# Performance work log

Measured on AMD Instinct MI355X. Metric: run time of the kernel, lower is better.

## Reference

```python
import jax, jax.numpy as jnp
import numpy as np

N_NODES = 50000
N_EDGES = 800000
N_GRAPHS = 64
PERIOD = 10
HID = 300
NLAYER = 5
EPS = 1e-5


def setup_inputs() -> dict:
    key = jax.random.key(0)
    ks = jax.random.split(key, 16)
    batch = jnp.sort(jax.random.randint(ks[0], (N_NODES,), 0, N_GRAPHS))
    x = jax.random.normal(ks[1], (N_NODES, 2 * PERIOD), dtype=jnp.float32)
    edge_index = jax.random.randint(ks[2], (2, N_EDGES), 0, N_NODES)
    edge_attr = jax.random.normal(ks[3], (N_EDGES,), dtype=jnp.float32)

    def xavier(k, fan_in, fan_out, shape):
        a = float(np.sqrt(6.0 / (fan_in + fan_out)))
        return jax.random.uniform(k, shape, jnp.float32, -a, a)

    linW = xavier(ks[4], 2 * PERIOD, HID, (2 * PERIOD, HID))
    linb = jnp.zeros((HID,), jnp.float32)
    W1s = xavier(ks[5], HID, 2 * HID, (NLAYER, HID, 2 * HID))
    b1s = jnp.zeros((NLAYER, 2 * HID), jnp.float32)
    g1s = jnp.ones((NLAYER, 2 * HID), jnp.float32)
    be1s = jnp.zeros((NLAYER, 2 * HID), jnp.float32)
    W2s = xavier(ks[6], 2 * HID, HID, (NLAYER, 2 * HID, HID))
    b2s = jnp.zeros((NLAYER, HID), jnp.float32)
    gos = jnp.ones((NLAYER, HID), jnp.float32)
    bos = jnp.zeros((NLAYER, HID), jnp.float32)
    return {"batch": batch, "x": x, "edge_index": edge_index, "edge_attr": edge_attr,
            "linW": linW, "linb": linb, "W1s": W1s, "b1s": b1s, "g1s": g1s,
            "be1s": be1s, "W2s": W2s, "b2s": b2s, "gos": gos, "bos": bos}


def _bn(h, g, b):
    # training-mode BatchNorm1d: batch mean, biased variance
    m = jnp.mean(h, axis=0)
    v = jnp.var(h, axis=0)
    return g * (h - m) * jax.lax.rsqrt(v + EPS) + b


def reference(batch, x, edge_index, edge_attr, linW, linb, W1s, b1s, g1s, be1s, W2s, b2s, gos, bos):
    src, dst = edge_index[0], edge_index[1]
    ew = edge_attr[:, None]  # [E,1]
    h = x @ linW + linb  # [N, HID]
    for i in range(NLAYER):
        # gather-modulate-scatter message passing (sign=False: message = w * x_j)
        msg = ew * h[src]  # [E, HID]
        agg = jax.ops.segment_sum(msg, dst, num_segments=N_NODES)  # [N, HID]
        # inner MLP with BatchNorm
        t = agg @ W1s[i] + b1s[i]  # [N, 2*HID]
        t = jax.nn.relu(_bn(t, g1s[i], be1s[i]))
        t = t @ W2s[i] + b2s[i]  # [N, HID]
        # outer BatchNorm
        h = _bn(t, gos[i], bos[i])
        if i != NLAYER - 1:
            h = jax.nn.relu(h)
    xpool = jax.ops.segment_sum(h, batch, num_segments=N_GRAPHS)  # [G, HID]
    return (h, xpool)
```

## Files before the change

kernel.cpp:

```cpp
#include <hip/hip_runtime.h>
#include <hip/hip_fp16.h>
#include <stdint.h>

typedef _Float16 f16x8 __attribute__((ext_vector_type(8)));
typedef unsigned short u16x8 __attribute__((ext_vector_type(8)));
typedef float f32x4 __attribute__((ext_vector_type(4)));

constexpr int NN  = 50000;
constexpr int NE  = 800000;
constexpr int NG  = 64;
constexpr int H   = 300;
constexpr int H2  = 600;
constexpr int IND = 20;
constexpr int NL  = 5;

constexpr int MP  = 50048;
constexpr int KP1 = 320;
constexpr int KP2 = 608;
constexpr int NP1 = 640;
constexpr int NP2 = 384;
constexpr int HCS = 320;

constexpr int SCAN_B = (NN + 1023) / 1024;

static __device__ __forceinline__ ushort f2h(float f) {
  return __half_as_ushort(__float2half(f));
}
static __device__ __forceinline__ float h2f_lo(uint32_t u) {
  return __half2float(__ushort_as_half((ushort)(u & 0xFFFFu)));
}
static __device__ __forceinline__ float h2f_hi(uint32_t u) {
  return __half2float(__ushort_as_half((ushort)(u >> 16)));
}
static __device__ __forceinline__ uint32_t packh(float a, float b) {
  return (uint32_t)f2h(a) | ((uint32_t)f2h(b) << 16);
}

static __device__ __forceinline__ f16x8 relu8(f16x8 t) {
#if __has_builtin(__builtin_elementwise_max)
  f16x8 z = 0;
  return __builtin_elementwise_max(t, z);
#else
  u16x8 u = *reinterpret_cast<u16x8*>(&t);
  u = u & (u16x8)((u >> 15) - (unsigned short)1);
  return *reinterpret_cast<f16x8*>(&u);
#endif
}


__global__ void hist_kernel(const int* __restrict__ dst, int* __restrict__ hist) {
  int i = blockIdx.x * blockDim.x + threadIdx.x;
  if (i < NE) atomicAdd(&hist[dst[i]], 1);
}

__global__ __launch_bounds__(1024) void scan1_kernel(const int* __restrict__ hist,
                                                     int* __restrict__ offs,
                                                     int* __restrict__ bsum) {
  __shared__ int sdata[1024];
  int b = blockIdx.x, tid = threadIdx.x;
  int i = b * 1024 + tid;
  int v = (i < NN) ? hist[i] : 0;
  sdata[tid] = v;
  __syncthreads();
  for (int ofs = 1; ofs < 1024; ofs <<= 1) {
    int t = (tid >= ofs) ? sdata[tid - ofs] : 0;
    __syncthreads();
    sdata[tid] += t;
    __syncthreads();
  }
  if (i < NN) offs[i] = sdata[tid] - v;
  if (tid == 1023) bsum[b] = sdata[1023];
}

__global__ void scan2_kernel(const int* __restrict__ bsum, int* __restrict__ bpre) {
  if (threadIdx.x == 0) {
    int run = 0;
    for (int b = 0; b < SCAN_B; ++b) {
      bpre[b] = run;
      run += bsum[b];
    }
    bpre[SCAN_B] = run;
  }
}

__global__ __launch_bounds__(1024) void scan3_kernel(const int* __restrict__ bpre,
                                                     int* __restrict__ offs,
                                                     int* __restrict__ cursor) {
  int b = blockIdx.x, tid = threadIdx.x;
  int i = b * 1024 + tid;
  if (i < NN) {
    int o = offs[i] + bpre[b];
    offs[i] = o;
    cursor[i] = o;
  }
  if (i == 0) offs[NN] = bpre[SCAN_B];
}

__global__ void scatter_kernel(const int* __restrict__ src, const int* __restrict__ dst,
                               const float* __restrict__ w, int* __restrict__ cursor,
                               int* __restrict__ ssrc, float* __restrict__ sw) {
  int i = blockIdx.x * blockDim.x + threadIdx.x;
  if (i < NE) {
    int d = dst[i];
    int p = atomicAdd(&cursor[d], 1);
    ssrc[p] = src[i];
    sw[p]   = w[i];
  }
}


__global__ void padzero_kernel(ushort* __restrict__ b, int KPAD, int Ntrue) {
  long long nA = (long long)(MP - NN) * KPAD;
  int padc = KPAD - Ntrue;
  long long nB = (long long)NN * padc;
  long long total = nA + nB;
  long long stride = (long long)gridDim.x * blockDim.x;
  for (long long i = blockIdx.x * (long long)blockDim.x + threadIdx.x; i < total; i += stride) {
    long long off;
    if (i < nA) {
      off = (long long)NN * KPAD + i;
    } else {
      long long j = i - nA;
      long long r = j / padc;
      long long c = Ntrue + (j - r * padc);
      off = r * KPAD + c;
    }
    b[off] = 0;
  }
}


__global__ void packW1_kernel(const float* __restrict__ W1s, ushort* __restrict__ Wp) {
  int idx = blockIdx.x * blockDim.x + threadIdx.x;
  if (idx >= NL * NP1 * KP1) return;
  int i = idx / (NP1 * KP1);
  int rem = idx - i * (NP1 * KP1);
  int n = rem / KP1;
  int k = rem - n * KP1;
  float v = (n < H2 && k < H) ? W1s[((long long)i * H + k) * H2 + n] : 0.f;
  Wp[idx] = f2h(v);
}

__global__ void packW2_kernel(const float* __restrict__ W2s, ushort* __restrict__ Wp) {
  int idx = blockIdx.x * blockDim.x + threadIdx.x;
  if (idx >= NL * NP2 * KP2) return;
  int i = idx / (NP2 * KP2);
  int rem = idx - i * (NP2 * KP2);
  int n = rem / KP2;
  int k = rem - n * KP2;
  float v = (n < H && k < H2) ? W2s[((long long)i * H2 + k) * H + n] : 0.f;
  Wp[idx] = f2h(v);
}


__global__ __launch_bounds__(256) void lin_kernel(const float* __restrict__ x,
                                                  const float* __restrict__ W,
                                                  const float* __restrict__ b,
                                                  ushort* __restrict__ hc) {
  __shared__ float Ws[IND * H];
  __shared__ float bs[H];
  int tid = threadIdx.x;
  for (int i = tid; i < IND * H; i += 256) Ws[i] = W[i];
  for (int i = tid; i < H; i += 256) bs[i] = b[i];
  __syncthreads();
  const int QPR = H / 4;
  int total = NN * QPR;
  for (int idx = blockIdx.x * 256 + tid; idx < total; idx += gridDim.x * 256) {
    int n = idx / QPR;
    int f = (idx - n * QPR) * 4;
    float a0 = bs[f], a1 = bs[f + 1], a2 = bs[f + 2], a3 = bs[f + 3];
    const float* xr = x + n * IND;
#pragma unroll
    for (int k = 0; k < IND; ++k) {
      float xv = xr[k];
      const float* wk = &Ws[k * H + f];
      a0 = fmaf(xv, wk[0], a0);
      a1 = fmaf(xv, wk[1], a1);
      a2 = fmaf(xv, wk[2], a2);
      a3 = fmaf(xv, wk[3], a3);
    }
    uint2 o = make_uint2(packh(a0, a1), packh(a2, a3));
    *reinterpret_cast<uint2*>(hc + (long long)n * HCS + f) = o;
  }
}


__global__ __launch_bounds__(192) void agg_kernel(const ushort* __restrict__ hc,
                                                  const int* __restrict__ offs,
                                                  const int* __restrict__ ssrc,
                                                  const float* __restrict__ sw,
                                                  ushort* __restrict__ agg) {
  int n = blockIdx.x;
  int t = threadIdx.x;
  if (t >= H / 2) return;
  int s = offs[n], e = offs[n + 1];
  float a0 = 0.f, a1 = 0.f;
  int i = s;
  for (; i + 7 < e; i += 8) {
    uint32_t u[8];
    float w[8];
#pragma unroll
    for (int j = 0; j < 8; ++j) {
      int sn = ssrc[i + j];
      w[j] = sw[i + j];
      u[j] = *reinterpret_cast<const uint32_t*>(hc + (long long)sn * HCS + 2 * t);
    }
#pragma unroll
    for (int j = 0; j < 8; ++j) {
      a0 = fmaf(w[j], h2f_lo(u[j]), a0);
      a1 = fmaf(w[j], h2f_hi(u[j]), a1);
    }
  }
  for (; i < e; ++i) {
    int sn = ssrc[i];
    float w = sw[i];
    uint32_t u = *reinterpret_cast<const uint32_t*>(hc + (long long)sn * HCS + 2 * t);
    a0 = fmaf(w, h2f_lo(u), a0);
    a1 = fmaf(w, h2f_hi(u), a1);
  }
  *reinterpret_cast<uint32_t*>(agg + (long long)n * KP1 + 2 * t) = packh(a0, a1);
}


template <bool FUSE_BN>
__global__ __launch_bounds__(256, 4) void gemm_mfma(
    const ushort* __restrict__ A, const ushort* __restrict__ Bp,
    const float* __restrict__ bias, ushort* __restrict__ C,
    float* __restrict__ sum, float* __restrict__ sq,
    int M, int Ntrue, int Ktiles, int KPAD, int Cstride, int ntiles,
    const ushort* __restrict__ bns, const ushort* __restrict__ bnh) {
  __shared__ ushort AL[2][128 * 32];
  int nwg = gridDim.x;
  int hw = blockIdx.x;
  int xcd = hw & 7, slot = hw >> 3;
  int q = nwg >> 3, r = nwg & 7;
  int logical = (xcd < r ? xcd * (q + 1) : r * (q + 1) + (xcd - r) * q) + slot;
  int mt = logical / ntiles;
  int nt = logical - mt * ntiles;

  int tid = threadIdx.x;
  int lane = tid & 63, wid = tid >> 6;
  int wm = wid >> 1, wn = wid & 1;
  int lm = lane & 15, lg = lane >> 4;
  long long bm = (long long)mt * 128;
  long long bn = (long long)nt * 128;

  int srow = lane >> 2;
  int slotc = lane & 3;

  const ushort* Bb = Bp + (bn + wn * 64 + lm) * KPAD + lg * 8;

  f32x4 acc[4][4] = {};

  auto stageA = [&](int buf, int kt) {
    int k0 = kt * 32;
#pragma unroll
    for (int j = 0; j < 2; ++j) {
      int row = j * 64 + wid * 16 + srow;
      int cg = slotc ^ ((row >> 1) & 3);
      long long go = (bm + row) * KPAD + k0 + cg * 8;
      ushort* l = &AL[buf][(j * 64 + wid * 16) * 32];
      __builtin_amdgcn_global_load_lds(
          (const __attribute__((address_space(1))) void*)(A + go),
          (__attribute__((address_space(3))) void*)l, 16, 0, 0);
    }
  };

  f16x8 bcur[4], bnxt[4];
  stageA(0, 0);
#pragma unroll
  for (int i = 0; i < 4; ++i)
    bcur[i] = *reinterpret_cast<const f16x8*>(Bb + (long long)i * 16 * KPAD);
  __syncthreads();

  for (int kt = 0; kt < Ktiles; ++kt) {
    int cur = kt & 1;
    int nk = kt + 1;
    if (nk < Ktiles) {
      stageA(nk & 1, nk);
#pragma unroll
      for (int i = 0; i < 4; ++i)
        bnxt[i] = *reinterpret_cast<const f16x8*>(Bb + (long long)i * 16 * KPAD + nk * 32);
    }
    f16x8 a[4];
#pragma unroll
    for (int i = 0; i < 4; ++i) {
      int row = wm * 64 + i * 16 + lm;
      int c = lg ^ ((row >> 1) & 3);
      a[i] = *reinterpret_cast<const f16x8*>(&AL[cur][row * 32 + c * 8]);
    }
    if constexpr (FUSE_BN) {
      int kbase = kt * 32 + lg * 8;
      f16x8 sv = *reinterpret_cast<const f16x8*>(bns + kbase);
      f16x8 hv = *reinterpret_cast<const f16x8*>(bnh + kbase);
#pragma unroll
      for (int i = 0; i < 4; ++i) a[i] = relu8(a[i] * sv + hv);
    }
#pragma unroll
    for (int mf = 0; mf < 4; ++mf)
#pragma unroll
      for (int nf = 0; nf < 4; ++nf)
        acc[mf][nf] = __builtin_amdgcn_mfma_f32_16x16x32_f16(a[mf], bcur[nf], acc[mf][nf], 0, 0, 0);
    __syncthreads();
#pragma unroll
    for (int i = 0; i < 4; ++i) bcur[i] = bnxt[i];
  }

  int colb = (int)bn + wn * 64 + lm;
#pragma unroll
  for (int nf = 0; nf < 4; ++nf) {
    int col = colb + nf * 16;
    bool cok = col < Ntrue;
    float bv = cok ? bias[col] : 0.f;
    float cs = 0.f, cq = 0.f;
#pragma unroll
    for (int mf = 0; mf < 4; ++mf) {
      int row0 = (int)bm + wm * 64 + mf * 16 + lg * 4;
      f32x4 v = acc[mf][nf];
#pragma unroll
      for (int e = 0; e < 4; ++e) {
        float w = v[e] + bv;
        bool ok = cok && (row0 + e < M);
        if (ok) {
          cs += w;
          cq = fmaf(w, w, cq);
        }
        float wp = __shfl_xor(w, 1);
        if (ok && ((lm & 1) == 0)) {
          *reinterpret_cast<uint32_t*>(&C[(long long)(row0 + e) * Cstride + col]) = packh(w, wp);
        }
      }
    }
    cs += __shfl_xor(cs, 16);
    cq += __shfl_xor(cq, 16);
    cs += __shfl_xor(cs, 32);
    cq += __shfl_xor(cq, 32);
    if (lg == 0 && cok) {
      atomicAdd(&sum[col], cs);
      atomicAdd(&sq[col], cq);
    }
  }
}


__global__ void finalize_kernel(const float* __restrict__ sum, const float* __restrict__ sq,
                                const float* __restrict__ g, const float* __restrict__ be,
                                int C, int Calloc, float invM, float* __restrict__ scale,
                                float* __restrict__ shift, ushort* __restrict__ scaleh,
                                ushort* __restrict__ shifth) {
  int c = blockIdx.x * blockDim.x + threadIdx.x;
  if (c >= Calloc) return;
  float sc = 0.f, sh = 0.f;
  if (c < C) {
    float m = sum[c] * invM;
    float v = sq[c] * invM - m * m;
    sc = g[c] * rsqrtf(v + 1e-5f);
    sh = be[c] - m * sc;
  }
  scale[c] = sc;
  shift[c] = sh;
  if (scaleh) {
    scaleh[c] = f2h(sc);
    shifth[c] = f2h(sh);
  }
}

template <bool LAST>
__global__ void bn2_kernel(const ushort* __restrict__ u_, const float* __restrict__ scale,
                           const float* __restrict__ shift, ushort* __restrict__ hc,
                           float* __restrict__ out) {
  const int QPR = H / 4;
  int total = NN * QPR;
  for (int idx = blockIdx.x * blockDim.x + threadIdx.x; idx < total;
       idx += gridDim.x * blockDim.x) {
    int r = idx / QPR;
    int c = (idx - r * QPR) * 4;
    uint2 u = *reinterpret_cast<const uint2*>(u_ + (long long)r * KP1 + c);
    float4 sc = *reinterpret_cast<const float4*>(scale + c);
    float4 sh = *reinterpret_cast<const float4*>(shift + c);
    float w0 = fmaf(h2f_lo(u.x), sc.x, sh.x);
    float w1 = fmaf(h2f_hi(u.x), sc.y, sh.y);
    float w2 = fmaf(h2f_lo(u.y), sc.z, sh.z);
    float w3 = fmaf(h2f_hi(u.y), sc.w, sh.w);
    if (LAST) {
      *reinterpret_cast<float4*>(out + (long long)r * H + c) = make_float4(w0, w1, w2, w3);
    } else {
      w0 = fmaxf(w0, 0.f);
      w1 = fmaxf(w1, 0.f);
      w2 = fmaxf(w2, 0.f);
      w3 = fmaxf(w3, 0.f);
      *reinterpret_cast<uint2*>(hc + (long long)r * HCS + c) =
          make_uint2(packh(w0, w1), packh(w2, w3));
    }
  }
}


__global__ void bounds_kernel(const int* __restrict__ batch, int* __restrict__ gstart) {
  int g = threadIdx.x;
  if (g > NG) return;
  if (g == NG) { gstart[NG] = NN; return; }
  int lo = 0, hi = NN;
  while (lo < hi) {
    int mid = (lo + hi) >> 1;
    if (batch[mid] < g) lo = mid + 1; else hi = mid;
  }
  gstart[g] = lo;
}

__global__ __launch_bounds__(320) void pool_kernel(const float* __restrict__ h,
                                                   const int* __restrict__ gstart,
                                                   float* __restrict__ xpool) {
  int g = blockIdx.x;
  int f = threadIdx.x;
  if (f >= H) return;
  int s = gstart[g], e = gstart[g + 1];
  float acc = 0.f;
  for (int r = s + blockIdx.y; r < e; r += gridDim.y) acc += h[(long long)r * H + f];
  atomicAdd(&xpool[g * H + f], acc);
}


extern "C" void kernel_launch(void* const* d_in, const int* in_sizes, int n_in,
                              void* d_out, int out_size, void* d_ws, size_t ws_size,
                              hipStream_t stream) {
  const int*   batch = (const int*)d_in[0];
  const float* x     = (const float*)d_in[1];
  const int*   eidx  = (const int*)d_in[2];
  const float* eattr = (const float*)d_in[3];
  const float* linW  = (const float*)d_in[4];
  const float* linb  = (const float*)d_in[5];
  const float* W1s   = (const float*)d_in[6];
  const float* b1s   = (const float*)d_in[7];
  const float* g1s   = (const float*)d_in[8];
  const float* be1s  = (const float*)d_in[9];
  const float* W2s   = (const float*)d_in[10];
  const float* b2s   = (const float*)d_in[11];
  const float* gos   = (const float*)d_in[12];
  const float* bos   = (const float*)d_in[13];

  const int* esrc = eidx;
  const int* edst = eidx + NE;

  char* p = (char*)d_ws;
  auto alloc = [&](size_t bytes) {
    char* r = p;
    p += (bytes + 255) & ~(size_t)255;
    return r;
  };
  ushort* tb   = (ushort*)alloc((size_t)MP * KP2 * 2);
  ushort* ub   = (ushort*)alloc((size_t)MP * KP1 * 2);
  ushort* hc   = (ushort*)alloc((size_t)NN * HCS * 2);
  ushort* W1p  = (ushort*)alloc((size_t)NL * NP1 * KP1 * 2);
  ushort* W2p  = (ushort*)alloc((size_t)NL * NP2 * KP2 * 2);
  int*    hist   = (int*)alloc((size_t)NN * 4);
  int*    offs   = (int*)alloc((size_t)(NN + 64) * 4);
  int*    cursor = (int*)alloc((size_t)NN * 4);
  int*    ssrc   = (int*)alloc((size_t)NE * 4);
  float*  sw     = (float*)alloc((size_t)NE * 4);
  int*    bsum   = (int*)alloc((size_t)(SCAN_B + 1) * 4);
  int*    bpre   = (int*)alloc((size_t)(SCAN_B + 1) * 4);
  float*  sum1   = (float*)alloc((size_t)(H2 * 2 + H * 2) * 4);
  float*  sq1    = sum1 + H2;
  float*  sum2   = sq1 + H2;
  float*  sq2    = sum2 + H;
  float*  scale1 = (float*)alloc((size_t)(KP2 * 2 + H * 2) * 4);
  float*  shift1 = scale1 + KP2;
  float*  scale2 = shift1 + KP2;
  float*  shift2 = scale2 + H;
  ushort* scaleh = (ushort*)alloc((size_t)KP2 * 2 * 2);
  ushort* shifth = scaleh + KP2;
  int*    gstart = (int*)alloc((size_t)(NG + 1) * 4);
  size_t needed = (size_t)(p - (char*)d_ws);
  if (ws_size < needed) return;

  float* hout  = (float*)d_out;
  float* xpool = hout + (long long)NN * H;

  padzero_kernel<<<1024, 256, 0, stream>>>(tb, KP2, H2);
  padzero_kernel<<<1024, 256, 0, stream>>>(ub, KP1, H);

  packW1_kernel<<<(NL * NP1 * KP1 + 255) / 256, 256, 0, stream>>>(W1s, W1p);
  packW2_kernel<<<(NL * NP2 * KP2 + 255) / 256, 256, 0, stream>>>(W2s, W2p);

  hipMemsetAsync(hist, 0, (size_t)NN * 4, stream);
  hist_kernel<<<(NE + 255) / 256, 256, 0, stream>>>(edst, hist);
  scan1_kernel<<<SCAN_B, 1024, 0, stream>>>(hist, offs, bsum);
  scan2_kernel<<<1, 64, 0, stream>>>(bsum, bpre);
  scan3_kernel<<<SCAN_B, 1024, 0, stream>>>(bpre, offs, cursor);
  scatter_kernel<<<(NE + 255) / 256, 256, 0, stream>>>(esrc, edst, eattr, cursor, ssrc, sw);

  lin_kernel<<<4096, 256, 0, stream>>>(x, linW, linb, hc);

  const int MT = MP / 128;
  for (int i = 0; i < NL; ++i) {
    agg_kernel<<<NN, 192, 0, stream>>>(hc, offs, ssrc, sw, ub);
    hipMemsetAsync(sum1, 0, (size_t)(H2 * 2 + H * 2) * 4, stream);

    gemm_mfma<false><<<MT * (NP1 / 128), 256, 0, stream>>>(
        ub, W1p + (size_t)i * NP1 * KP1, b1s + (size_t)i * H2, tb,
        sum1, sq1, NN, H2, KP1 / 32, KP1, KP2, NP1 / 128, nullptr, nullptr);
    finalize_kernel<<<(KP2 + 255) / 256, 256, 0, stream>>>(
        sum1, sq1, g1s + (size_t)i * H2, be1s + (size_t)i * H2, H2, KP2, 1.f / NN,
        scale1, shift1, scaleh, shifth);

    gemm_mfma<true><<<MT * (NP2 / 128), 256, 0, stream>>>(
        tb, W2p + (size_t)i * NP2 * KP2, b2s + (size_t)i * H, ub,
        sum2, sq2, NN, H, KP2 / 32, KP2, KP1, NP2 / 128, scaleh, shifth);
    finalize_kernel<<<(H + 255) / 256, 256, 0, stream>>>(
        sum2, sq2, gos + (size_t)i * H, bos + (size_t)i * H, H, H, 1.f / NN,
        scale2, shift2, nullptr, nullptr);
    if (i < NL - 1) {
      bn2_kernel<false><<<4096, 256, 0, stream>>>(ub, scale2, shift2, hc, hout);
    } else {
      bn2_kernel<true><<<4096, 256, 0, stream>>>(ub, scale2, shift2, hc, hout);
    }
  }

  hipMemsetAsync(xpool, 0, (size_t)NG * H * 4, stream);
  bounds_kernel<<<1, 128, 0, stream>>>(batch, gstart);
  pool_kernel<<<dim3(NG, 8), 320, 0, stream>>>(hout, gstart, xpool);
}
```

Measured before the change: 1.354 ms.

## Switch MFMA GEMM to single-wave 64x64 tiles without workgroup barriers

The fused GEMM kernel moves from a 256-thread workgroup computing a 128x128 tile to a single 64-thread wave computing a 64x64 tile, launched on a correspondingly larger grid. Because each workgroup is one wave, the __syncthreads calls are dropped and explicit s_waitcnt vmcnt instructions order the async global-to-LDS A loads. The register double-buffering of B is removed, so B fragments are loaded in the same iteration they are consumed. This removes barrier stalls and raises the number of independent workgroups, but A tiles are no longer shared across waves through LDS, and B load latency is less hidden.

```diff
diff --git a/kernel.cpp b/kernel.cpp
--- a/kernel.cpp
+++ b/kernel.cpp
@@ -223,13 +223,13 @@
 
 
 template <bool FUSE_BN>
-__global__ __launch_bounds__(256, 4) void gemm_mfma(
+__global__ __launch_bounds__(64, 4) void gemm_mfma(
     const ushort* __restrict__ A, const ushort* __restrict__ Bp,
     const float* __restrict__ bias, ushort* __restrict__ C,
     float* __restrict__ sum, float* __restrict__ sq,
     int M, int Ntrue, int Ktiles, int KPAD, int Cstride, int ntiles,
     const ushort* __restrict__ bns, const ushort* __restrict__ bnh) {
-  __shared__ ushort AL[2][128 * 32];
+  __shared__ ushort AL[2][64 * 32];
   int nwg = gridDim.x;
   int hw = blockIdx.x;
   int xcd = hw & 7, slot = hw >> 3;
@@ -238,54 +238,51 @@
   int mt = logical / ntiles;
   int nt = logical - mt * ntiles;
 
-  int tid = threadIdx.x;
-  int lane = tid & 63, wid = tid >> 6;
-  int wm = wid >> 1, wn = wid & 1;
+  int lane = threadIdx.x & 63;
   int lm = lane & 15, lg = lane >> 4;
-  long long bm = (long long)mt * 128;
-  long long bn = (long long)nt * 128;
+  long long bm = (long long)mt * 64;
+  long long bn = (long long)nt * 64;
 
   int srow = lane >> 2;
   int slotc = lane & 3;
 
-  const ushort* Bb = Bp + (bn + wn * 64 + lm) * KPAD + lg * 8;
+  const ushort* Bb = Bp + (bn + lm) * KPAD + lg * 8;
 
   f32x4 acc[4][4] = {};
 
   auto stageA = [&](int buf, int kt) {
     int k0 = kt * 32;
 #pragma unroll
-    for (int j = 0; j < 2; ++j) {
-      int row = j * 64 + wid * 16 + srow;
+    for (int j = 0; j < 4; ++j) {
+      int row = j * 16 + srow;
       int cg = slotc ^ ((row >> 1) & 3);
       long long go = (bm + row) * KPAD + k0 + cg * 8;
-      ushort* l = &AL[buf][(j * 64 + wid * 16) * 32];
+      ushort* l = &AL[buf][(j * 16) * 32];
       __builtin_amdgcn_global_load_lds(
           (const __attribute__((address_space(1))) void*)(A + go),
           (__attribute__((address_space(3))) void*)l, 16, 0, 0);
     }
   };
 
-  f16x8 bcur[4], bnxt[4];
   stageA(0, 0);
-#pragma unroll
-  for (int i = 0; i < 4; ++i)
-    bcur[i] = *reinterpret_cast<const f16x8*>(Bb + (long long)i * 16 * KPAD);
-  __syncthreads();
 
   for (int kt = 0; kt < Ktiles; ++kt) {
     int cur = kt & 1;
     int nk = kt + 1;
+    f16x8 b[4];
+#pragma unroll
+    for (int i = 0; i < 4; ++i)
+      b[i] = *reinterpret_cast<const f16x8*>(Bb + (long long)i * 16 * KPAD + kt * 32);
     if (nk < Ktiles) {
       stageA(nk & 1, nk);
-#pragma unroll
-      for (int i = 0; i < 4; ++i)
-        bnxt[i] = *reinterpret_cast<const f16x8*>(Bb + (long long)i * 16 * KPAD + nk * 32);
+      asm volatile("s_waitcnt vmcnt(4)" ::: "memory");
+    } else {
+      asm volatile("s_waitcnt vmcnt(0)" ::: "memory");
     }
     f16x8 a[4];
 #pragma unroll
     for (int i = 0; i < 4; ++i) {
-      int row = wm * 64 + i * 16 + lm;
+      int row = i * 16 + lm;
       int c = lg ^ ((row >> 1) & 3);
       a[i] = *reinterpret_cast<const f16x8*>(&AL[cur][row * 32 + c * 8]);
     }
@@ -300,13 +297,10 @@
     for (int mf = 0; mf < 4; ++mf)
 #pragma unroll
       for (int nf = 0; nf < 4; ++nf)
-        acc[mf][nf] = __builtin_amdgcn_mfma_f32_16x16x32_f16(a[mf], bcur[nf], acc[mf][nf], 0, 0, 0);
-    __syncthreads();
-#pragma unroll
-    for (int i = 0; i < 4; ++i) bcur[i] = bnxt[i];
-  }
-
-  int colb = (int)bn + wn * 64 + lm;
+        acc[mf][nf] = __builtin_amdgcn_mfma_f32_16x16x32_f16(a[mf], b[nf], acc[mf][nf], 0, 0, 0);
+  }
+
+  int colb = (int)bn + lm;
 #pragma unroll
   for (int nf = 0; nf < 4; ++nf) {
     int col = colb + nf * 16;
@@ -315,7 +309,7 @@
     float cs = 0.f, cq = 0.f;
 #pragma unroll
     for (int mf = 0; mf < 4; ++mf) {
-      int row0 = (int)bm + wm * 64 + mf * 16 + lg * 4;
+      int row0 = (int)bm + mf * 16 + lg * 4;
       f32x4 v = acc[mf][nf];
 #pragma unroll
       for (int e = 0; e < 4; ++e) {
@@ -492,21 +486,21 @@
 
   lin_kernel<<<4096, 256, 0, stream>>>(x, linW, linb, hc);
 
-  const int MT = MP / 128;
+  const int MT = MP / 64;
   for (int i = 0; i < NL; ++i) {
     agg_kernel<<<NN, 192, 0, stream>>>(hc, offs, ssrc, sw, ub);
     hipMemsetAsync(sum1, 0, (size_t)(H2 * 2 + H * 2) * 4, stream);
 
-    gemm_mfma<false><<<MT * (NP1 / 128), 256, 0, stream>>>(
+    gemm_mfma<false><<<MT * (NP1 / 64), 64, 0, stream>>>(
         ub, W1p + (size_t)i * NP1 * KP1, b1s + (size_t)i * H2, tb,
-        sum1, sq1, NN, H2, KP1 / 32, KP1, KP2, NP1 / 128, nullptr, nullptr);
+        sum1, sq1, NN, H2, KP1 / 32, KP1, KP2, NP1 / 64, nullptr, nullptr);
     finalize_kernel<<<(KP2 + 255) / 256, 256, 0, stream>>>(
         sum1, sq1, g1s + (size_t)i * H2, be1s + (size_t)i * H2, H2, KP2, 1.f / NN,
         scale1, shift1, scaleh, shifth);
 
-    gemm_mfma<true><<<MT * (NP2 / 128), 256, 0, stream>>>(
+    gemm_mfma<true><<<MT * (NP2 / 64), 64, 0, stream>>>(
         tb, W2p + (size_t)i * NP2 * KP2, b2s + (size_t)i * H, ub,
-        sum2, sq2, NN, H, KP2 / 32, KP2, KP1, NP2 / 128, scaleh, shifth);
+        sum2, sq2, NN, H, KP2 / 32, KP2, KP1, NP2 / 64, scaleh, shifth);
     finalize_kernel<<<(H + 255) / 256, 256, 0, stream>>>(
         sum2, sq2, gos + (size_t)i * H, bos + (size_t)i * H, H, H, 1.f / NN,
         scale2, shift2, nullptr, nullptr);
```

New measurement: 1.377 ms. Within noise of the previous version (+1.7%).

## Stage full-K A panel in LDS once per block with 64-row tiles

Applied to the files above, without the earlier changes.

The GEMM now uses 64x128 tiles with two waves per block, each covering 64 columns. The whole 64-row A panel across all of K goes into dynamic LDS with one up-front async load and an XOR swizzle. This removes the per-K-tile A staging, double buffering and per-iteration barriers. In exchange each block uses much more LDS (about 40-78 KB), which lowers occupancy, and the load of A is no longer overlapped with compute, so the loop relies on B prefetch and more resident blocks to hide latency.

```diff
diff --git a/kernel.cpp b/kernel.cpp
--- a/kernel.cpp
+++ b/kernel.cpp
@@ -223,13 +223,13 @@
 
 
 template <bool FUSE_BN>
-__global__ __launch_bounds__(256, 4) void gemm_mfma(
+__global__ __launch_bounds__(128, 2) void gemm_mfma(
     const ushort* __restrict__ A, const ushort* __restrict__ Bp,
     const float* __restrict__ bias, ushort* __restrict__ C,
     float* __restrict__ sum, float* __restrict__ sq,
     int M, int Ntrue, int Ktiles, int KPAD, int Cstride, int ntiles,
     const ushort* __restrict__ bns, const ushort* __restrict__ bnh) {
-  __shared__ ushort AL[2][128 * 32];
+  extern __shared__ ushort AL[];
   int nwg = gridDim.x;
   int hw = blockIdx.x;
   int xcd = hw & 7, slot = hw >> 3;
@@ -240,44 +240,38 @@
 
   int tid = threadIdx.x;
   int lane = tid & 63, wid = tid >> 6;
-  int wm = wid >> 1, wn = wid & 1;
   int lm = lane & 15, lg = lane >> 4;
-  long long bm = (long long)mt * 128;
+  long long bm = (long long)mt * 64;
   long long bn = (long long)nt * 128;
 
-  int srow = lane >> 2;
-  int slotc = lane & 3;
-
-  const ushort* Bb = Bp + (bn + wn * 64 + lm) * KPAD + lg * 8;
+  const int CPR = KPAD >> 3;
+  const int CPRA = CPR & ~7;
+  const int CH = 64 * CPR;
+
+  const ushort* At = A + bm * KPAD;
+  for (int p0 = wid * 64; p0 < CH; p0 += 128) {
+    int p = p0 + lane;
+    int row = p / CPR;
+    int c = p - row * CPR;
+    int sc = (c < CPRA) ? (c ^ (row & 7)) : c;
+    __builtin_amdgcn_global_load_lds(
+        (const __attribute__((address_space(1))) void*)(At + (long long)(row * CPR + sc) * 8),
+        (__attribute__((address_space(3))) void*)(AL + (long long)p0 * 8), 16, 0, 0);
+  }
+
+  const ushort* Bb = Bp + (bn + wid * 64 + lm) * KPAD + lg * 8;
 
   f32x4 acc[4][4] = {};
-
-  auto stageA = [&](int buf, int kt) {
-    int k0 = kt * 32;
-#pragma unroll
-    for (int j = 0; j < 2; ++j) {
-      int row = j * 64 + wid * 16 + srow;
-      int cg = slotc ^ ((row >> 1) & 3);
-      long long go = (bm + row) * KPAD + k0 + cg * 8;
-      ushort* l = &AL[buf][(j * 64 + wid * 16) * 32];
-      __builtin_amdgcn_global_load_lds(
-          (const __attribute__((address_space(1))) void*)(A + go),
-          (__attribute__((address_space(3))) void*)l, 16, 0, 0);
-    }
-  };
-
   f16x8 bcur[4], bnxt[4];
-  stageA(0, 0);
 #pragma unroll
   for (int i = 0; i < 4; ++i)
     bcur[i] = *reinterpret_cast<const f16x8*>(Bb + (long long)i * 16 * KPAD);
+
   __syncthreads();
 
   for (int kt = 0; kt < Ktiles; ++kt) {
-    int cur = kt & 1;
     int nk = kt + 1;
     if (nk < Ktiles) {
-      stageA(nk & 1, nk);
 #pragma unroll
       for (int i = 0; i < 4; ++i)
         bnxt[i] = *reinterpret_cast<const f16x8*>(Bb + (long long)i * 16 * KPAD + nk * 32);
@@ -285,9 +279,10 @@
     f16x8 a[4];
 #pragma unroll
     for (int i = 0; i < 4; ++i) {
-      int row = wm * 64 + i * 16 + lm;
-      int c = lg ^ ((row >> 1) & 3);
-      a[i] = *reinterpret_cast<const f16x8*>(&AL[cur][row * 32 + c * 8]);
+      int row = i * 16 + lm;
+      int c = kt * 4 + lg;
+      int sc = (c < CPRA) ? (c ^ (row & 7)) : c;
+      a[i] = *reinterpret_cast<const f16x8*>(AL + row * KPAD + sc * 8);
     }
     if constexpr (FUSE_BN) {
       int kbase = kt * 32 + lg * 8;
@@ -301,12 +296,11 @@
 #pragma unroll
       for (int nf = 0; nf < 4; ++nf)
         acc[mf][nf] = __builtin_amdgcn_mfma_f32_16x16x32_f16(a[mf], bcur[nf], acc[mf][nf], 0, 0, 0);
-    __syncthreads();
 #pragma unroll
     for (int i = 0; i < 4; ++i) bcur[i] = bnxt[i];
   }
 
-  int colb = (int)bn + wn * 64 + lm;
+  int colb = (int)bn + wid * 64 + lm;
 #pragma unroll
   for (int nf = 0; nf < 4; ++nf) {
     int col = colb + nf * 16;
@@ -315,7 +309,7 @@
     float cs = 0.f, cq = 0.f;
 #pragma unroll
     for (int mf = 0; mf < 4; ++mf) {
-      int row0 = (int)bm + wm * 64 + mf * 16 + lg * 4;
+      int row0 = (int)bm + mf * 16 + lg * 4;
       f32x4 v = acc[mf][nf];
 #pragma unroll
       for (int e = 0; e < 4; ++e) {
@@ -492,19 +486,21 @@
 
   lin_kernel<<<4096, 256, 0, stream>>>(x, linW, linb, hc);
 
-  const int MT = MP / 128;
+  const int MT = MP / 64;
+  const size_t lds1 = (size_t)64 * KP1 * 2;
+  const size_t lds2 = (size_t)64 * KP2 * 2;
   for (int i = 0; i < NL; ++i) {
     agg_kernel<<<NN, 192, 0, stream>>>(hc, offs, ssrc, sw, ub);
     hipMemsetAsync(sum1, 0, (size_t)(H2 * 2 + H * 2) * 4, stream);
 
-    gemm_mfma<false><<<MT * (NP1 / 128), 256, 0, stream>>>(
+    gemm_mfma<false><<<MT * (NP1 / 128), 128, lds1, stream>>>(
         ub, W1p + (size_t)i * NP1 * KP1, b1s + (size_t)i * H2, tb,
         sum1, sq1, NN, H2, KP1 / 32, KP1, KP2, NP1 / 128, nullptr, nullptr);
     finalize_kernel<<<(KP2 + 255) / 256, 256, 0, stream>>>(
         sum1, sq1, g1s + (size_t)i * H2, be1s + (size_t)i * H2, H2, KP2, 1.f / NN,
         scale1, shift1, scaleh, shifth);
 
-    gemm_mfma<true><<<MT * (NP2 / 128), 256, 0, stream>>>(
+    gemm_mfma<true><<<MT * (NP2 / 128), 128, lds2, stream>>>(
         tb, W2p + (size_t)i * NP2 * KP2, b2s + (size_t)i * H, ub,
         sum2, sq2, NN, H, KP2 / 32, KP2, KP1, NP2 / 128, scaleh, shifth);
     finalize_kernel<<<(H + 255) / 256, 256, 0, stream>>>(
```

After: 1.556 ms. 1.15x slower.
